# Kernel optimization log

Hardware: AMD Instinct MI355X
Metric: run time of the kernel (lower is better)

Reference implementation:

```python
import jax, jax.numpy as jnp
import numpy as np

N = 30000        # nodes
E = 480000       # edges
IN = 256         # input feature dim
D = 32           # num_hidden per head
H = 4            # heads for layers 0,1
C = 47           # num_classes (final layer, 1 head)
NEG_SLOPE = 0.2


def setup_inputs() -> dict:
    key = jax.random.key(0)
    ks = jax.random.split(key, 16)
    def glorot(k, shape):
        fan = sum(shape)
        return jax.random.normal(k, shape, jnp.float32) * jnp.sqrt(2.0 / fan)
    inp = {
        "x": jax.random.normal(ks[0], (N, IN), jnp.float32),
        # layer 0: IN -> H*D, no residual
        "W0": glorot(ks[1], (IN, H * D)),
        "al0": glorot(ks[2], (H, D)),
        "ar0": glorot(ks[3], (H, D)),
        # layer 1: H*D -> H*D, residual fc
        "W1": glorot(ks[4], (H * D, H * D)),
        "resW1": glorot(ks[5], (H * D, H * D)),
        "al1": glorot(ks[6], (H, D)),
        "ar1": glorot(ks[7], (H, D)),
        # final layer: H*D -> 1*C, residual fc
        "W2": glorot(ks[8], (H * D, 1 * C)),
        "resW2": glorot(ks[9], (H * D, 1 * C)),
        "al2": glorot(ks[10], (1, C)),
        "ar2": glorot(ks[11], (1, C)),
        "src": jax.random.randint(ks[12], (E,), 0, N, jnp.int32),
        "dst": jax.random.randint(ks[13], (E,), 0, N, jnp.int32),
    }
    return inp


def gat_layer(h, W, al, ar, src, dst, heads, d, resW=None, act=None):
    # h: [N, F_in]; W: [F_in, heads*d]; al/ar: [heads, d]
    n = h.shape[0]
    feat = (h @ W).reshape(n, heads, d)                 # [N, H, D]
    el = (feat * al).sum(-1)                            # [N, H]
    er = (feat * ar).sum(-1)                            # [N, H]
    e = jax.nn.leaky_relu(el[src] + er[dst], NEG_SLOPE)  # [E, H]
    # edge softmax over incoming edges of each dst node (numerically stable)
    emax = jax.ops.segment_max(e, dst, num_segments=n)  # [N, H]
    emax = jnp.where(jnp.isfinite(emax), emax, 0.0)     # guard empty segments
    w = jnp.exp(e - emax[dst])                          # [E, H]
    wsum = jax.ops.segment_sum(w, dst, num_segments=n)  # [N, H]
    a = w / jnp.maximum(wsum[dst], 1e-9)                # [E, H]
    msg = feat[src] * a[:, :, None]                     # [E, H, D]
    rst = jax.ops.segment_sum(msg, dst, num_segments=n)  # [N, H, D]
    if resW is not None:
        rst = rst + (h @ resW).reshape(n, heads, d)
    if act is not None:
        rst = act(rst)
    return rst, e


def reference(x, W0, al0, ar0, W1, resW1, al1, ar1, W2, resW2, al2, ar2, src, dst):
    act = jax.nn.elu
    # layer 0 (no residual, no in-conv activation), then flatten + activation
    h, e0 = gat_layer(x, W0, al0, ar0, src, dst, H, D)
    h = act(h.reshape(N, H * D))
    # layer 1 (residual, in-conv activation), then flatten + activation
    h, e1 = gat_layer(h, W1, al1, ar1, src, dst, H, D, resW=resW1, act=act)
    h = act(h.reshape(N, H * D))
    # final layer (residual, no activation), mean over heads
    h, e2 = gat_layer(h, W2, al2, ar2, src, dst, 1, C, resW=resW2)
    logits = h.mean(axis=1)                             # [N, C]
    return (logits, e0, e1, e2)
```

## Files before the change

### kernel.cpp

```cpp
#include <hip/hip_runtime.h>
#include <hip/hip_bf16.h>
#include <math.h>

#define NN 30000
#define NE 480000
#define FIN 256
#define DH 32
#define NH 4
#define NC 47
#define NODE_BLKS 7500
#define EDGE_BLKS 1875
#define SCAN_CHUNK 1024
#define NCHUNKS 30

typedef __attribute__((ext_vector_type(8))) short frag_ab;
typedef __attribute__((ext_vector_type(4))) float f32x4;
typedef __hip_bfloat16 bf16;

static inline size_t align256(size_t x) { return (x + 255) & ~(size_t)255; }

__device__ __forceinline__ short f2bf(float f) {
    union { float f; unsigned u; } c; c.f = f;
    unsigned r = (c.u + 0x7FFFu + ((c.u >> 16) & 1u)) >> 16;
    return (short)r;
}
__device__ __forceinline__ float b2f(unsigned short u) {
    union { unsigned u; float f; } c; c.u = (unsigned)u << 16; return c.f;
}
__device__ __forceinline__ float expw(float v) {
    return __expf((v >= 0.f) ? v : 0.2f * v);
}
__device__ __forceinline__ float lrelu(float v) {
    return (v >= 0.f) ? v : 0.2f * v;
}

__global__ void prep_count(const float* __restrict__ W0, const float* __restrict__ W1,
                           const float* __restrict__ rW1, const float* __restrict__ W2,
                           const float* __restrict__ rW2,
                           const float* __restrict__ al0, const float* __restrict__ ar0,
                           const float* __restrict__ al1, const float* __restrict__ ar1,
                           const float* __restrict__ al2, const float* __restrict__ ar2,
                           bf16* __restrict__ W0t, bf16* __restrict__ W1t,
                           bf16* __restrict__ rW1t, bf16* __restrict__ W2t,
                           bf16* __restrict__ rW2t,
                           const int* __restrict__ dst, int* __restrict__ cursor) {
    if (blockIdx.y == 5) {
        int e = blockIdx.x * 256 + threadIdx.x;
        if (e < NE) atomicAdd(&cursor[dst[e]], 1);
        return;
    }
    const float *W, *al, *ar; bf16* Wt; int K, M, rows, H, D;
    switch (blockIdx.y) {
        case 0: W = W0;  Wt = W0t;  K = 256; M = 128; rows = 144; H = 4; D = 32; al = al0; ar = ar0; break;
        case 1: W = W1;  Wt = W1t;  K = 128; M = 128; rows = 144; H = 4; D = 32; al = al1; ar = ar1; break;
        case 2: W = rW1; Wt = rW1t; K = 128; M = 128; rows = 128; H = 0; D = 0;  al = nullptr; ar = nullptr; break;
        case 3: W = W2;  Wt = W2t;  K = 128; M = 47;  rows = 64;  H = 1; D = 47; al = al2; ar = ar2; break;
        default: W = rW2; Wt = rW2t; K = 128; M = 47; rows = 48;  H = 0; D = 0;  al = nullptr; ar = nullptr; break;
    }
    int i = blockIdx.x * 256 + threadIdx.x;
    if (i >= rows * K) return;
    int row = i / K, k = i - row * K;
    float v = 0.f;
    if (row < M) {
        v = W[(long)k * M + row];
    } else if (H > 0 && row < M + 2 * H) {
        int idx = row - M;
        int h = (idx < H) ? idx : idx - H;
        const float* a = (idx < H) ? al : ar;
        float s = 0.f;
        for (int d = 0; d < D; ++d) s += W[(long)k * M + h * D + d] * a[h * D + d];
        v = s;
    }
    Wt[i] = __float2bfloat16(v);
}

__global__ __launch_bounds__(256) void scanB(const int* __restrict__ bsum,
                                             int* __restrict__ offs,
                                             int* __restrict__ cursor) {
    __shared__ int bases[NCHUNKS + 1];
    if (threadIdx.x == 0) {
        int acc = 0;
        for (int j = 0; j < NCHUNKS; ++j) { bases[j] = acc; acc += bsum[j]; }
        bases[NCHUNKS] = acc;
    }
    __syncthreads();
    const int i = blockIdx.x * 256 + threadIdx.x;
    if (i < NN) {
        const int o = offs[i] + bases[i >> 10];
        offs[i] = o;
        cursor[i] = o;
    }
    if (i == 0) offs[NN] = bases[NCHUNKS];
}

__global__ void fill_k(const int* __restrict__ dst, const int* __restrict__ src,
                       int* __restrict__ cursor, int* __restrict__ srcs, int E) {
    int e = blockIdx.x * blockDim.x + threadIdx.x;
    if (e < E) {
        int p = atomicAdd(&cursor[dst[e]], 1);
        srcs[p] = src[e];
    }
}

template <bool A_F32, int NT1, int NT2, int HH, int TAIL>
__global__ __launch_bounds__(256) void gemm_mfma(
    const void* __restrict__ Av, const bf16* __restrict__ B1t,
    const bf16* __restrict__ B2t,
    bf16* __restrict__ C1b, float* __restrict__ el, float* __restrict__ er,
    float* __restrict__ C2, int N, int K, int M, int nGemmBlocks,
    const int* __restrict__ t_cnt, int* __restrict__ t_offs, int* __restrict__ t_bsum,
    const float4* __restrict__ pel, const float4* __restrict__ per,
    const int* __restrict__ src, const int* __restrict__ dst,
    float* __restrict__ eout) {
    constexpr int LP = 56;
    __shared__ bf16 As[64][LP];
    __shared__ bf16 Bs1[NT1 * 16][LP];
    __shared__ bf16 Bs2[(NT2 > 0) ? NT2 * 16 : 1][LP];
    __shared__ int ws4[4];

    const int tid = threadIdx.x;

    if constexpr (TAIL == 1) {
        if (blockIdx.x >= nGemmBlocks) {
            const int chunk = blockIdx.x - nGemmBlocks;
            const int lane = tid & 63;
            const int wid = tid >> 6;
            const int g = chunk * SCAN_CHUNK + tid * 4;
            const int a0 = (g + 0 < NN) ? t_cnt[g + 0] : 0;
            const int a1 = (g + 1 < NN) ? t_cnt[g + 1] : 0;
            const int a2 = (g + 2 < NN) ? t_cnt[g + 2] : 0;
            const int a3 = (g + 3 < NN) ? t_cnt[g + 3] : 0;
            const int lsum = a0 + a1 + a2 + a3;
            int x = lsum;
            #pragma unroll
            for (int off = 1; off < 64; off <<= 1) {
                int y = __shfl_up(x, off);
                if (lane >= off) x += y;
            }
            if (lane == 63) ws4[wid] = x;
            __syncthreads();
            int wbase = 0;
            #pragma unroll
            for (int j = 0; j < 4; ++j) if (j < wid) wbase += ws4[j];
            const int excl = wbase + x - lsum;
            if (g + 0 < NN) t_offs[g + 0] = excl;
            if (g + 1 < NN) t_offs[g + 1] = excl + a0;
            if (g + 2 < NN) t_offs[g + 2] = excl + a0 + a1;
            if (g + 3 < NN) t_offs[g + 3] = excl + a0 + a1 + a2;
            if (tid == 0) t_bsum[chunk] = ws4[0] + ws4[1] + ws4[2] + ws4[3];
            return;
        }
    }
    if constexpr (TAIL == 2) {
        if (blockIdx.x >= nGemmBlocks) {
            const int e = (blockIdx.x - nGemmBlocks) * 256 + tid;
            const int s = src[e], d = dst[e];
            const float4 a = pel[s], b = per[d];
            float4 v;
            v.x = lrelu(a.x + b.x); v.y = lrelu(a.y + b.y);
            v.z = lrelu(a.z + b.z); v.w = lrelu(a.w + b.w);
            *reinterpret_cast<float4*>(eout + e * 4) = v;
            return;
        }
    }

    const int lane = tid & 63;
    const int wid = tid >> 6;
    const int row0 = blockIdx.x * 64;
    const int l15 = lane & 15;
    const int kq = lane >> 4;

    f32x4 acc1[NT1], acc2[(NT2 > 0) ? NT2 : 1];
    #pragma unroll
    for (int t = 0; t < NT1; ++t) acc1[t] = (f32x4){0.f, 0.f, 0.f, 0.f};
    if constexpr (NT2 > 0) {
        #pragma unroll
        for (int t = 0; t < NT2; ++t) acc2[t] = (f32x4){0.f, 0.f, 0.f, 0.f};
    }

    for (int k0 = 0; k0 < K; k0 += 32) {
        {
            const int r = tid >> 2, kk = (tid & 3) * 8;
            const int gr = row0 + r;
            if constexpr (A_F32) {
                const float* A = (const float*)Av;
                short tmp[8];
                if (gr < N) {
                    const float4 v0 = *(const float4*)&A[(long)gr * K + k0 + kk];
                    const float4 v1 = *(const float4*)&A[(long)gr * K + k0 + kk + 4];
                    tmp[0] = f2bf(v0.x); tmp[1] = f2bf(v0.y); tmp[2] = f2bf(v0.z); tmp[3] = f2bf(v0.w);
                    tmp[4] = f2bf(v1.x); tmp[5] = f2bf(v1.y); tmp[6] = f2bf(v1.z); tmp[7] = f2bf(v1.w);
                } else {
                    #pragma unroll
                    for (int j = 0; j < 8; ++j) tmp[j] = 0;
                }
                *(frag_ab*)&As[r][kk] = *(const frag_ab*)tmp;
            } else {
                const bf16* A = (const bf16*)Av;
                frag_ab v = {0, 0, 0, 0, 0, 0, 0, 0};
                if (gr < N) v = *(const frag_ab*)&A[(long)gr * K + k0 + kk];
                *(frag_ab*)&As[r][kk] = v;
            }
        }
        for (int i = tid; i < NT1 * 64; i += 256) {
            const int c = i >> 2, kk = (i & 3) * 8;
            *(frag_ab*)&Bs1[c][kk] = *(const frag_ab*)&B1t[(long)c * K + k0 + kk];
        }
        if constexpr (NT2 > 0) {
            for (int i = tid; i < NT2 * 64; i += 256) {
                const int c = i >> 2, kk = (i & 3) * 8;
                *(frag_ab*)&Bs2[c][kk] = *(const frag_ab*)&B2t[(long)c * K + k0 + kk];
            }
        }
        __syncthreads();

        const frag_ab a = *(const frag_ab*)&As[wid * 16 + l15][kq * 8];
        #pragma unroll
        for (int t = 0; t < NT1; ++t) {
            const frag_ab b = *(const frag_ab*)&Bs1[t * 16 + l15][kq * 8];
            acc1[t] = __builtin_amdgcn_mfma_f32_16x16x32_bf16(a, b, acc1[t], 0, 0, 0);
        }
        if constexpr (NT2 > 0) {
            #pragma unroll
            for (int t = 0; t < NT2; ++t) {
                const frag_ab b = *(const frag_ab*)&Bs2[t * 16 + l15][kq * 8];
                acc2[t] = __builtin_amdgcn_mfma_f32_16x16x32_bf16(a, b, acc2[t], 0, 0, 0);
            }
        }
        __syncthreads();
    }

    const int r0 = row0 + wid * 16 + kq * 4;
    #pragma unroll
    for (int t = 0; t < NT1; ++t) {
        const int c = t * 16 + l15;
        #pragma unroll
        for (int reg = 0; reg < 4; ++reg) {
            const int r = r0 + reg;
            if (r >= N) continue;
            const float v = acc1[t][reg];
            if (c < M) {
                C1b[(long)r * M + c] = __float2bfloat16(v);
            } else if (c < M + HH) {
                el[(long)r * HH + (c - M)] = v;
            } else if (c < M + 2 * HH) {
                er[(long)r * HH + (c - M - HH)] = v;
            }
        }
    }
    if constexpr (NT2 > 0) {
        #pragma unroll
        for (int t = 0; t < NT2; ++t) {
            const int c = t * 16 + l15;
            if (c >= M) continue;
            #pragma unroll
            for (int reg = 0; reg < 4; ++reg) {
                const int r = r0 + reg;
                if (r < N) C2[(long)r * M + c] = acc2[t][reg];
            }
        }
    }
}

template <int NELU, bool HAS_RES>
__global__ __launch_bounds__(256) void node_agg4(
    const bf16* __restrict__ featb, const float4* __restrict__ el4,
    const float4* __restrict__ er4, float4* __restrict__ es4,
    const int* __restrict__ offs, const int* __restrict__ srcs,
    const float* __restrict__ res, bf16* __restrict__ out) {
    __shared__ float4 sc[4][64];
    const int node = (int)((blockIdx.x * blockDim.x + threadIdx.x) >> 6);
    const int lane = threadIdx.x & 63;
    const int wid = threadIdx.x >> 6;
    const int beg = offs[node], end = offs[node + 1];
    const float4 ern = er4[node];

    float4 s4 = make_float4(0.f, 0.f, 0.f, 0.f);
    for (int i = beg + lane; i < end; i += 64) {
        const float4 elv = el4[srcs[i]];
        float4 t;
        t.x = expw(elv.x + ern.x); t.y = expw(elv.y + ern.y);
        t.z = expw(elv.z + ern.z); t.w = expw(elv.w + ern.w);
        s4.x += t.x; s4.y += t.y; s4.z += t.z; s4.w += t.w;
        const int idx = i - beg;
        if (idx < 64) sc[wid][idx] = t;
        else es4[i] = t;
    }
    #pragma unroll
    for (int off = 32; off > 0; off >>= 1) {
        s4.x += __shfl_xor(s4.x, off);
        s4.y += __shfl_xor(s4.y, off);
        s4.z += __shfl_xor(s4.z, off);
        s4.w += __shfl_xor(s4.w, off);
    }
    __syncthreads();

    const int q = lane >> 4;
    const int l15 = lane & 15;
    const int fi = l15 * 8;
    const int h = l15 >> 2;
    const float sh = (h == 0) ? s4.x : (h == 1) ? s4.y : (h == 2) ? s4.z : s4.w;
    const float inv = 1.f / fmaxf(sh, 1e-9f);
    const float* esf = (const float*)es4;
    const float* scf = (const float*)sc[wid];

    float a[8] = {0.f, 0.f, 0.f, 0.f, 0.f, 0.f, 0.f, 0.f};
    int i = beg + q;
    for (; i + 4 < end; i += 8) {
        const int iB = i + 4;
        const int idxA = i - beg, idxB = iB - beg;
        const int snA = srcs[i], snB = srcs[iB];
        const float wA = (idxA < 64) ? scf[idxA * 4 + h] : esf[i * 4 + h];
        const float wB = (idxB < 64) ? scf[idxB * 4 + h] : esf[iB * 4 + h];
        const frag_ab fA = *(const frag_ab*)(featb + (long)snA * 128 + fi);
        const frag_ab fB = *(const frag_ab*)(featb + (long)snB * 128 + fi);
        #pragma unroll
        for (int j = 0; j < 8; ++j)
            a[j] += wA * b2f((unsigned short)fA[j]) + wB * b2f((unsigned short)fB[j]);
    }
    for (; i < end; i += 4) {
        const int idx = i - beg;
        const int sn = srcs[i];
        const float w = (idx < 64) ? scf[idx * 4 + h] : esf[i * 4 + h];
        const frag_ab f = *(const frag_ab*)(featb + (long)sn * 128 + fi);
        #pragma unroll
        for (int j = 0; j < 8; ++j) a[j] += w * b2f((unsigned short)f[j]);
    }
    #pragma unroll
    for (int j = 0; j < 8; ++j) {
        a[j] += __shfl_xor(a[j], 16);
        a[j] += __shfl_xor(a[j], 32);
    }

    if (lane < 16) {
        float v[8];
        #pragma unroll
        for (int j = 0; j < 8; ++j) v[j] = a[j] * inv;
        if constexpr (HAS_RES) {
            const float4 r0 = *(const float4*)(res + (long)node * 128 + fi);
            const float4 r1 = *(const float4*)(res + (long)node * 128 + fi + 4);
            v[0] += r0.x; v[1] += r0.y; v[2] += r0.z; v[3] += r0.w;
            v[4] += r1.x; v[5] += r1.y; v[6] += r1.z; v[7] += r1.w;
        }
        #pragma unroll
        for (int t = 0; t < NELU; ++t)
            #pragma unroll
            for (int j = 0; j < 8; ++j)
                v[j] = (v[j] > 0.f) ? v[j] : expm1f(v[j]);
        frag_ab o;
        #pragma unroll
        for (int j = 0; j < 8; ++j) o[j] = f2bf(v[j]);
        *(frag_ab*)(out + (long)node * 128 + fi) = o;
    }
}

__global__ __launch_bounds__(256) void final_k(
    const bf16* __restrict__ featb, const float* __restrict__ el2s,
    const float* __restrict__ er2s, float* __restrict__ es1,
    const int* __restrict__ offs, const int* __restrict__ srcs,
    const float* __restrict__ res, float* __restrict__ logits,
    const int* __restrict__ src, const int* __restrict__ dst,
    float* __restrict__ e2) {
    __shared__ float sc1[4][64];
    if (blockIdx.x < NODE_BLKS) {
        const int node = (int)((blockIdx.x * blockDim.x + threadIdx.x) >> 6);
        const int lane = threadIdx.x & 63;
        const int wid = threadIdx.x >> 6;
        const int beg = offs[node], end = offs[node + 1];
        const float ern = er2s[node];

        float s = 0.f;
        for (int i = beg + lane; i < end; i += 64) {
            const float t = expw(el2s[srcs[i]] + ern);
            s += t;
            const int idx = i - beg;
            if (idx < 64) sc1[wid][idx] = t;
            else es1[i] = t;
        }
        #pragma unroll
        for (int off = 32; off > 0; off >>= 1) s += __shfl_xor(s, off);
        const float inv = 1.f / fmaxf(s, 1e-9f);
        __syncthreads();

        const bool active = lane < NC;
        float acc = 0.f;
        int i = beg;
        for (; i + 8 <= end; i += 8) {
            const int d0 = i - beg;
            int sn[8]; float w[8];
            #pragma unroll
            for (int k = 0; k < 8; ++k) {
                sn[k] = srcs[i + k];
                w[k] = (d0 + k < 64) ? sc1[wid][d0 + k] : es1[i + k];
            }
            if (active) {
                #pragma unroll
                for (int k = 0; k < 8; ++k)
                    acc += w[k] * __bfloat162float(featb[(long)sn[k] * NC + lane]);
            }
        }
        for (; i < end; ++i) {
            const int idx = i - beg;
            const float w = (idx < 64) ? sc1[wid][idx] : es1[i];
            if (active) acc += w * __bfloat162float(featb[(long)srcs[i] * NC + lane]);
        }
        if (active) {
            logits[(long)node * NC + lane] = acc * inv + res[(long)node * NC + lane];
        }
    } else {
        const int e = (blockIdx.x - NODE_BLKS) * 256 + threadIdx.x;
        e2[e] = lrelu(el2s[src[e]] + er2s[dst[e]]);
    }
}

extern "C" void kernel_launch(void* const* d_in, const int* in_sizes, int n_in,
                              void* d_out, int out_size, void* d_ws, size_t ws_size,
                              hipStream_t stream) {
    const float* x     = (const float*)d_in[0];
    const float* W0    = (const float*)d_in[1];
    const float* al0   = (const float*)d_in[2];
    const float* ar0   = (const float*)d_in[3];
    const float* W1    = (const float*)d_in[4];
    const float* resW1 = (const float*)d_in[5];
    const float* al1   = (const float*)d_in[6];
    const float* ar1   = (const float*)d_in[7];
    const float* W2    = (const float*)d_in[8];
    const float* resW2 = (const float*)d_in[9];
    const float* al2   = (const float*)d_in[10];
    const float* ar2   = (const float*)d_in[11];
    const int*   src   = (const int*)d_in[12];
    const int*   dst   = (const int*)d_in[13];

    float* out    = (float*)d_out;
    float* logits = out;
    float* e0     = out + (long)NN * NC;
    float* e1     = e0 + (long)NE * NH;
    float* e2     = e1 + (long)NE * NH;

    char* p = (char*)d_ws;
    int* offs   = (int*)p; p += align256(sizeof(int) * (NN + 1));
    int* cursor = (int*)p; p += align256(sizeof(int) * NN);
    int* bsum   = (int*)p; p += align256(sizeof(int) * 32);
    int* srcs   = (int*)p; p += align256(sizeof(int) * NE);
    float* el0b = (float*)p; p += align256(sizeof(float) * NN * NH);
    float* er0b = (float*)p; p += align256(sizeof(float) * NN * NH);
    float* el1b = (float*)p; p += align256(sizeof(float) * NN * NH);
    float* er1b = (float*)p; p += align256(sizeof(float) * NN * NH);
    float* el2b = (float*)p; p += align256(sizeof(float) * NN);
    float* er2b = (float*)p; p += align256(sizeof(float) * NN);
    float* es   = (float*)p; p += align256(sizeof(float) * (long)NE * NH);
    float* resb = (float*)p; p += align256(sizeof(float) * (long)NN * 128);
    bf16* featb = (bf16*)p; p += align256(sizeof(bf16) * (long)NN * 128);
    bf16* hb    = (bf16*)p; p += align256(sizeof(bf16) * (long)NN * 128);
    bf16* W0t   = (bf16*)p; p += align256(sizeof(bf16) * 144 * 256);
    bf16* W1t   = (bf16*)p; p += align256(sizeof(bf16) * 144 * 128);
    bf16* rW1t  = (bf16*)p; p += align256(sizeof(bf16) * 128 * 128);
    bf16* W2t   = (bf16*)p; p += align256(sizeof(bf16) * 64 * 128);
    bf16* rW2t  = (bf16*)p; p += align256(sizeof(bf16) * 48 * 128);

    const int gemmBlocks = (NN + 63) / 64;

    hipMemsetAsync(cursor, 0, sizeof(int) * NN, stream);
    prep_count<<<dim3(EDGE_BLKS, 6), 256, 0, stream>>>(
        W0, W1, resW1, W2, resW2, al0, ar0, al1, ar1, al2, ar2,
        W0t, W1t, rW1t, W2t, rW2t, dst, cursor);

    gemm_mfma<true, 9, 0, NH, 1><<<gemmBlocks + NCHUNKS, 256, 0, stream>>>(
        x, W0t, nullptr, featb, el0b, er0b, nullptr, NN, FIN, 128, gemmBlocks,
        cursor, offs, bsum, nullptr, nullptr, nullptr, nullptr, nullptr);

    scanB<<<(NN + 255) / 256, 256, 0, stream>>>(bsum, offs, cursor);
    fill_k<<<EDGE_BLKS, 256, 0, stream>>>(dst, src, cursor, srcs, NE);

    node_agg4<1, false><<<NODE_BLKS, 256, 0, stream>>>(
        featb, (const float4*)el0b, (const float4*)er0b, (float4*)es, offs, srcs, nullptr, hb);

    gemm_mfma<false, 9, 8, NH, 2><<<gemmBlocks + EDGE_BLKS, 256, 0, stream>>>(
        hb, W1t, rW1t, featb, el1b, er1b, resb, NN, 128, 128, gemmBlocks,
        nullptr, nullptr, nullptr,
        (const float4*)el0b, (const float4*)er0b, src, dst, e0);

    node_agg4<2, true><<<NODE_BLKS, 256, 0, stream>>>(
        featb, (const float4*)el1b, (const float4*)er1b, (float4*)es, offs, srcs, resb, hb);

    gemm_mfma<false, 4, 3, 1, 2><<<gemmBlocks + EDGE_BLKS, 256, 0, stream>>>(
        hb, W2t, rW2t, featb, el2b, er2b, resb, NN, 128, NC, gemmBlocks,
        nullptr, nullptr, nullptr,
        (const float4*)el1b, (const float4*)er1b, src, dst, e1);

    final_k<<<NODE_BLKS + EDGE_BLKS, 256, 0, stream>>>(
        featb, el2b, er2b, es, offs, srcs, resb, logits, src, dst, e2);
}
```

Before: 201.7 us.

## Drop scan kernel and fill atomics via edge ranks; store residual in bf16

```diff
diff --git a/kernel.cpp b/kernel.cpp
--- a/kernel.cpp
+++ b/kernel.cpp
@@ -43,10 +43,11 @@
                            bf16* __restrict__ W0t, bf16* __restrict__ W1t,
                            bf16* __restrict__ rW1t, bf16* __restrict__ W2t,
                            bf16* __restrict__ rW2t,
-                           const int* __restrict__ dst, int* __restrict__ cursor) {
+                           const int* __restrict__ dst, int* __restrict__ cnt,
+                           int* __restrict__ rank) {
     if (blockIdx.y == 5) {
         int e = blockIdx.x * 256 + threadIdx.x;
-        if (e < NE) atomicAdd(&cursor[dst[e]], 1);
+        if (e < NE) rank[e] = atomicAdd(&cnt[dst[e]], 1);
         return;
     }
     const float *W, *al, *ar; bf16* Wt; int K, M, rows, H, D;
@@ -74,31 +75,13 @@
     Wt[i] = __float2bfloat16(v);
 }
 
-__global__ __launch_bounds__(256) void scanB(const int* __restrict__ bsum,
-                                             int* __restrict__ offs,
-                                             int* __restrict__ cursor) {
-    __shared__ int bases[NCHUNKS + 1];
-    if (threadIdx.x == 0) {
-        int acc = 0;
-        for (int j = 0; j < NCHUNKS; ++j) { bases[j] = acc; acc += bsum[j]; }
-        bases[NCHUNKS] = acc;
-    }
-    __syncthreads();
-    const int i = blockIdx.x * 256 + threadIdx.x;
-    if (i < NN) {
-        const int o = offs[i] + bases[i >> 10];
-        offs[i] = o;
-        cursor[i] = o;
-    }
-    if (i == 0) offs[NN] = bases[NCHUNKS];
-}
-
 __global__ void fill_k(const int* __restrict__ dst, const int* __restrict__ src,
-                       int* __restrict__ cursor, int* __restrict__ srcs, int E) {
+                       const int* __restrict__ rank, const int* __restrict__ loff,
+                       const int* __restrict__ bases, int* __restrict__ srcs) {
     int e = blockIdx.x * blockDim.x + threadIdx.x;
-    if (e < E) {
-        int p = atomicAdd(&cursor[dst[e]], 1);
-        srcs[p] = src[e];
+    if (e < NE) {
+        const int d = dst[e];
+        srcs[loff[d] + bases[d >> 10] + rank[e]] = src[e];
     }
 }
 
@@ -107,8 +90,9 @@
     const void* __restrict__ Av, const bf16* __restrict__ B1t,
     const bf16* __restrict__ B2t,
     bf16* __restrict__ C1b, float* __restrict__ el, float* __restrict__ er,
-    float* __restrict__ C2, int N, int K, int M, int nGemmBlocks,
-    const int* __restrict__ t_cnt, int* __restrict__ t_offs, int* __restrict__ t_bsum,
+    bf16* __restrict__ C2, int N, int K, int M, int nGemmBlocks,
+    const int* __restrict__ t_cnt, int* __restrict__ t_loff, int* __restrict__ t_bsum,
+    int* __restrict__ t_bases, int* __restrict__ t_done,
     const float4* __restrict__ pel, const float4* __restrict__ per,
     const int* __restrict__ src, const int* __restrict__ dst,
     float* __restrict__ eout) {
@@ -143,11 +127,21 @@
             #pragma unroll
             for (int j = 0; j < 4; ++j) if (j < wid) wbase += ws4[j];
             const int excl = wbase + x - lsum;
-            if (g + 0 < NN) t_offs[g + 0] = excl;
-            if (g + 1 < NN) t_offs[g + 1] = excl + a0;
-            if (g + 2 < NN) t_offs[g + 2] = excl + a0 + a1;
-            if (g + 3 < NN) t_offs[g + 3] = excl + a0 + a1 + a2;
-            if (tid == 0) t_bsum[chunk] = ws4[0] + ws4[1] + ws4[2] + ws4[3];
+            if (g + 0 < NN) t_loff[g + 0] = excl;
+            if (g + 1 < NN) t_loff[g + 1] = excl + a0;
+            if (g + 2 < NN) t_loff[g + 2] = excl + a0 + a1;
+            if (g + 3 < NN) t_loff[g + 3] = excl + a0 + a1 + a2;
+            if (tid == 0) {
+                t_bsum[chunk] = ws4[0] + ws4[1] + ws4[2] + ws4[3];
+                __threadfence();
+                const int prev = atomicAdd(t_done, 1);
+                if (prev == NCHUNKS - 1) {
+                    __threadfence();
+                    int acc = 0;
+                    for (int j = 0; j < NCHUNKS; ++j) { t_bases[j] = acc; acc += t_bsum[j]; }
+                    t_bases[NCHUNKS] = acc;
+                }
+            }
             return;
         }
     }
@@ -256,7 +250,7 @@
             #pragma unroll
             for (int reg = 0; reg < 4; ++reg) {
                 const int r = r0 + reg;
-                if (r < N) C2[(long)r * M + c] = acc2[t][reg];
+                if (r < N) C2[(long)r * M + c] = __float2bfloat16(acc2[t][reg]);
             }
         }
     }
@@ -266,13 +260,15 @@
 __global__ __launch_bounds__(256) void node_agg4(
     const bf16* __restrict__ featb, const float4* __restrict__ el4,
     const float4* __restrict__ er4, float4* __restrict__ es4,
-    const int* __restrict__ offs, const int* __restrict__ srcs,
-    const float* __restrict__ res, bf16* __restrict__ out) {
+    const int* __restrict__ loff, const int* __restrict__ bases,
+    const int* __restrict__ srcs,
+    const bf16* __restrict__ res, bf16* __restrict__ out) {
     __shared__ float4 sc[4][64];
     const int node = (int)((blockIdx.x * blockDim.x + threadIdx.x) >> 6);
     const int lane = threadIdx.x & 63;
     const int wid = threadIdx.x >> 6;
-    const int beg = offs[node], end = offs[node + 1];
+    const int beg = loff[node] + bases[node >> 10];
+    const int end = (node == NN - 1) ? NE : loff[node + 1] + bases[(node + 1) >> 10];
     const float4 ern = er4[node];
 
     float4 s4 = make_float4(0.f, 0.f, 0.f, 0.f);
@@ -337,10 +333,9 @@
         #pragma unroll
         for (int j = 0; j < 8; ++j) v[j] = a[j] * inv;
         if constexpr (HAS_RES) {
-            const float4 r0 = *(const float4*)(res + (long)node * 128 + fi);
-            const float4 r1 = *(const float4*)(res + (long)node * 128 + fi + 4);
-            v[0] += r0.x; v[1] += r0.y; v[2] += r0.z; v[3] += r0.w;
-            v[4] += r1.x; v[5] += r1.y; v[6] += r1.z; v[7] += r1.w;
+            const frag_ab rr = *(const frag_ab*)(res + (long)node * 128 + fi);
+            #pragma unroll
+            for (int j = 0; j < 8; ++j) v[j] += b2f((unsigned short)rr[j]);
         }
         #pragma unroll
         for (int t = 0; t < NELU; ++t)
@@ -357,8 +352,9 @@
 __global__ __launch_bounds__(256) void final_k(
     const bf16* __restrict__ featb, const float* __restrict__ el2s,
     const float* __restrict__ er2s, float* __restrict__ es1,
-    const int* __restrict__ offs, const int* __restrict__ srcs,
-    const float* __restrict__ res, float* __restrict__ logits,
+    const int* __restrict__ loff, const int* __restrict__ bases,
+    const int* __restrict__ srcs,
+    const bf16* __restrict__ res, float* __restrict__ logits,
     const int* __restrict__ src, const int* __restrict__ dst,
     float* __restrict__ e2) {
     __shared__ float sc1[4][64];
@@ -366,7 +362,8 @@
         const int node = (int)((blockIdx.x * blockDim.x + threadIdx.x) >> 6);
         const int lane = threadIdx.x & 63;
         const int wid = threadIdx.x >> 6;
-        const int beg = offs[node], end = offs[node + 1];
+        const int beg = loff[node] + bases[node >> 10];
+        const int end = (node == NN - 1) ? NE : loff[node + 1] + bases[(node + 1) >> 10];
         const float ern = er2s[node];
 
         float s = 0.f;
@@ -405,7 +402,8 @@
             if (active) acc += w * __bfloat162float(featb[(long)srcs[i] * NC + lane]);
         }
         if (active) {
-            logits[(long)node * NC + lane] = acc * inv + res[(long)node * NC + lane];
+            logits[(long)node * NC + lane] =
+                acc * inv + __bfloat162float(res[(long)node * NC + lane]);
         }
     } else {
         const int e = (blockIdx.x - NODE_BLKS) * 256 + threadIdx.x;
@@ -438,9 +436,12 @@
     float* e2     = e1 + (long)NE * NH;
 
     char* p = (char*)d_ws;
-    int* offs   = (int*)p; p += align256(sizeof(int) * (NN + 1));
-    int* cursor = (int*)p; p += align256(sizeof(int) * NN);
+    int* cnt    = (int*)p; p += align256(sizeof(int) * (NN + 64));
+    int* done   = cnt + NN;
+    int* loff   = (int*)p; p += align256(sizeof(int) * (NN + 1));
     int* bsum   = (int*)p; p += align256(sizeof(int) * 32);
+    int* bases  = (int*)p; p += align256(sizeof(int) * 32);
+    int* rank   = (int*)p; p += align256(sizeof(int) * NE);
     int* srcs   = (int*)p; p += align256(sizeof(int) * NE);
     float* el0b = (float*)p; p += align256(sizeof(float) * NN * NH);
     float* er0b = (float*)p; p += align256(sizeof(float) * NN * NH);
@@ -449,7 +450,7 @@
     float* el2b = (float*)p; p += align256(sizeof(float) * NN);
     float* er2b = (float*)p; p += align256(sizeof(float) * NN);
     float* es   = (float*)p; p += align256(sizeof(float) * (long)NE * NH);
-    float* resb = (float*)p; p += align256(sizeof(float) * (long)NN * 128);
+    bf16* resb  = (bf16*)p; p += align256(sizeof(bf16) * (long)NN * 128);
     bf16* featb = (bf16*)p; p += align256(sizeof(bf16) * (long)NN * 128);
     bf16* hb    = (bf16*)p; p += align256(sizeof(bf16) * (long)NN * 128);
     bf16* W0t   = (bf16*)p; p += align256(sizeof(bf16) * 144 * 256);
@@ -460,34 +461,35 @@
 
     const int gemmBlocks = (NN + 63) / 64;
 
-    hipMemsetAsync(cursor, 0, sizeof(int) * NN, stream);
+    hipMemsetAsync(cnt, 0, sizeof(int) * (NN + 64), stream);
     prep_count<<<dim3(EDGE_BLKS, 6), 256, 0, stream>>>(
         W0, W1, resW1, W2, resW2, al0, ar0, al1, ar1, al2, ar2,
-        W0t, W1t, rW1t, W2t, rW2t, dst, cursor);
+        W0t, W1t, rW1t, W2t, rW2t, dst, cnt, rank);
 
     gemm_mfma<true, 9, 0, NH, 1><<<gemmBlocks + NCHUNKS, 256, 0, stream>>>(
         x, W0t, nullptr, featb, el0b, er0b, nullptr, NN, FIN, 128, gemmBlocks,
-        cursor, offs, bsum, nullptr, nullptr, nullptr, nullptr, nullptr);
-
-    scanB<<<(NN + 255) / 256, 256, 0, stream>>>(bsum, offs, cursor);
-    fill_k<<<EDGE_BLKS, 256, 0, stream>>>(dst, src, cursor, srcs, NE);
+        cnt, loff, bsum, bases, done, nullptr, nullptr, nullptr, nullptr, nullptr);
+
+    fill_k<<<EDGE_BLKS, 256, 0, stream>>>(dst, src, rank, loff, bases, srcs);
 
     node_agg4<1, false><<<NODE_BLKS, 256, 0, stream>>>(
-        featb, (const float4*)el0b, (const float4*)er0b, (float4*)es, offs, srcs, nullptr, hb);
+        featb, (const float4*)el0b, (const float4*)er0b, (float4*)es,
+        loff, bases, srcs, nullptr, hb);
 
     gemm_mfma<false, 9, 8, NH, 2><<<gemmBlocks + EDGE_BLKS, 256, 0, stream>>>(
         hb, W1t, rW1t, featb, el1b, er1b, resb, NN, 128, 128, gemmBlocks,
-        nullptr, nullptr, nullptr,
+        nullptr, nullptr, nullptr, nullptr, nullptr,
         (const float4*)el0b, (const float4*)er0b, src, dst, e0);
 
     node_agg4<2, true><<<NODE_BLKS, 256, 0, stream>>>(
-        featb, (const float4*)el1b, (const float4*)er1b, (float4*)es, offs, srcs, resb, hb);
+        featb, (const float4*)el1b, (const float4*)er1b, (float4*)es,
+        loff, bases, srcs, resb, hb);
 
     gemm_mfma<false, 4, 3, 1, 2><<<gemmBlocks + EDGE_BLKS, 256, 0, stream>>>(
         hb, W2t, rW2t, featb, el2b, er2b, resb, NN, 128, NC, gemmBlocks,
-        nullptr, nullptr, nullptr,
+        nullptr, nullptr, nullptr, nullptr, nullptr,
         (const float4*)el1b, (const float4*)er1b, src, dst, e1);
 
     final_k<<<NODE_BLKS + EDGE_BLKS, 256, 0, stream>>>(
-        featb, el2b, er2b, es, offs, srcs, resb, logits, src, dst, e2);
-}
+        featb, el2b, er2b, es, loff, bases, srcs, resb, logits, src, dst, e2);
+}
```

After: 182.5 us. 1.1x faster.
